# Kernel optimization log

Hardware: AMD Instinct MI355X
Metric: run time of the kernel (lower is better)

Reference implementation:

```python
import jax, jax.numpy as jnp
import numpy as np

EPS = 1e-6

def _feature_map(x):
    # elu(x) + 1 == where(x>0, x+1, exp(x))
    return jax.nn.elu(x) + 1.0

def setup_inputs() -> dict:
    key = jax.random.key(0)
    kq, kk, kv, km = jax.random.split(key, 4)
    B, H, S, D = 4, 16, 4096, 64
    query = jax.random.normal(kq, (B, H, S, D), dtype=jnp.float32)
    key_t = jax.random.normal(kk, (B, H, S, D), dtype=jnp.float32)
    value = jax.random.normal(kv, (B, H, S, D), dtype=jnp.float32)
    # True = padded position
    key_padding_mask = jax.random.bernoulli(km, 0.25, (B, S))
    return {"query": query, "key": key_t, "value": value,
            "key_padding_mask": key_padding_mask}

def reference(query, key, value, key_padding_mask):
    q = _feature_map(query)              # [B,H,S,D]
    k = _feature_map(key)
    v = value
    # valid = ~mask, broadcast over heads and feature dim
    valid = (~key_padding_mask)[:, None, :, None].astype(query.dtype)  # [B,1,S,1]
    k = k * valid
    v = v * valid
    kv = jnp.einsum('bhsd,bhsf->bhdf', k, v)              # [B,H,D,D]
    z = jnp.einsum('bhtd,bhd->bht', q, k.sum(axis=2)) + EPS
    out = jnp.einsum('bhtd,bhdf->bhtf', q, kv) / z[..., None]
    return out
```

## Files before the change

kernel.cpp:

```cpp
#include <hip/hip_runtime.h>

#define S_LEN 4096
#define D_DIM 64
#define NBH   64
#define EPS_F 1e-6f
#define PSZ   (D_DIM * D_DIM + D_DIM)

__device__ __forceinline__ float phi_f(float x) {
    return x > 0.0f ? x + 1.0f : __expf(x);
}

__global__ void detect_mask(const unsigned int* __restrict__ w,
                            unsigned int* __restrict__ flag) {
    __shared__ int all01, allf;
    if (threadIdx.x == 0) { all01 = 1; allf = 1; }
    __syncthreads();
    int a = 1, f = 1;
    for (int i = threadIdx.x; i < 4096; i += blockDim.x) {
        unsigned int v = w[i];
        if (v > 1u) a = 0;
        if (v != 0u && v != 0x3F800000u) f = 0;
    }
    if (!a) atomicExch(&all01, 0);
    if (!f) atomicExch(&allf, 0);
    __syncthreads();
    if (threadIdx.x == 0) *flag = all01 ? 0u : (allf ? 2u : 1u);
}

__global__ __launch_bounds__(256) void la_phase1(
    const float* __restrict__ K, const float* __restrict__ V,
    const void* __restrict__ mask, const unsigned int* __restrict__ flagp,
    float* __restrict__ partials, int CH)
{
    __shared__ float smem[2 * 32 * 64];
    __shared__ float ksred[4][64];

    const int bh   = blockIdx.x;
    const int b    = bh >> 4;
    const unsigned int flag = *flagp;
    const int tid  = threadIdx.x;
    const int wave = tid >> 6;
    const int lane = tid & 63;
    const int tt   = lane >> 3;
    const int tf   = lane & 7;
    const int chunk = S_LEN / CH;
    const int NT    = chunk / 32;
    const int s0    = blockIdx.y * chunk;

    const float* Kbh = K + (size_t)bh * S_LEN * D_DIM;
    const float* Vbh = V + (size_t)bh * S_LEN * D_DIM;
    const int*           mi = (const int*)mask;
    const unsigned char* mb = (const unsigned char*)mask;
    const float*         mf = (const float*)mask;

    float acc[8][8];
    float ks[8];
    #pragma unroll
    for (int i = 0; i < 8; ++i) {
        ks[i] = 0.0f;
        #pragma unroll
        for (int j = 0; j < 8; ++j) acc[i][j] = 0.0f;
    }

    const int row0 = tid >> 4;
    const int col0 = (tid & 15) * 4;

    float4 kr[2], vr[2];
    int    pr[2];

    auto issue = [&](int ts) {
        #pragma unroll
        for (int p = 0; p < 2; ++p) {
            int row = p * 16 + row0;
            int s   = s0 + ts + row;
            int ml  = b * S_LEN + s;
            bool pad;
            if (flag == 0u)      pad = (mi[ml] != 0);
            else if (flag == 1u) pad = (mb[ml] != 0);
            else                 pad = (mf[ml] != 0.0f);
            pr[p] = pad ? 1 : 0;
            kr[p] = *reinterpret_cast<const float4*>(&Kbh[(size_t)s * D_DIM + col0]);
            vr[p] = *reinterpret_cast<const float4*>(&Vbh[(size_t)s * D_DIM + col0]);
        }
    };

    issue(0);
    for (int it = 0; it < NT; ++it) {
        #pragma unroll
        for (int p = 0; p < 2; ++p) {
            int row = p * 16 + row0;
            float4 k4 = kr[p], v4 = vr[p];
            if (pr[p]) {
                k4 = make_float4(0.f, 0.f, 0.f, 0.f);
                v4 = make_float4(0.f, 0.f, 0.f, 0.f);
            } else {
                k4.x = phi_f(k4.x); k4.y = phi_f(k4.y);
                k4.z = phi_f(k4.z); k4.w = phi_f(k4.w);
            }
            *reinterpret_cast<float4*>(&smem[row * 64 + col0])        = k4;
            *reinterpret_cast<float4*>(&smem[2048 + row * 64 + col0]) = v4;
        }
        __syncthreads();
        if (it + 1 < NT) issue((it + 1) * 32);
        #pragma unroll
        for (int r = 0; r < 8; ++r) {
            const int row = wave * 8 + r;
            float kk[8], vv[8];
            *reinterpret_cast<float4*>(&kk[0]) = *reinterpret_cast<const float4*>(&smem[row * 64 + tt * 8]);
            *reinterpret_cast<float4*>(&kk[4]) = *reinterpret_cast<const float4*>(&smem[row * 64 + tt * 8 + 4]);
            *reinterpret_cast<float4*>(&vv[0]) = *reinterpret_cast<const float4*>(&smem[2048 + row * 64 + tf * 8]);
            *reinterpret_cast<float4*>(&vv[4]) = *reinterpret_cast<const float4*>(&smem[2048 + row * 64 + tf * 8 + 4]);
            #pragma unroll
            for (int i = 0; i < 8; ++i) {
                #pragma unroll
                for (int j = 0; j < 8; ++j)
                    acc[i][j] = fmaf(kk[i], vv[j], acc[i][j]);
                ks[i] += kk[i];
            }
        }
        __syncthreads();
    }

    if (tf == 0) {
        #pragma unroll
        for (int i = 0; i < 8; ++i) ksred[wave][tt * 8 + i] = ks[i];
    }
    for (int w = 0; w < 4; ++w) {
        if (wave == w) {
            #pragma unroll
            for (int i = 0; i < 8; ++i) {
                float4* p0 = reinterpret_cast<float4*>(&smem[(tt * 8 + i) * 64 + tf * 8]);
                float4 a0 = make_float4(acc[i][0], acc[i][1], acc[i][2], acc[i][3]);
                float4 a1 = make_float4(acc[i][4], acc[i][5], acc[i][6], acc[i][7]);
                if (w == 0) { p0[0] = a0; p0[1] = a1; }
                else {
                    float4 c0 = p0[0], c1 = p0[1];
                    c0.x += a0.x; c0.y += a0.y; c0.z += a0.z; c0.w += a0.w;
                    c1.x += a1.x; c1.y += a1.y; c1.z += a1.z; c1.w += a1.w;
                    p0[0] = c0; p0[1] = c1;
                }
            }
        }
        __syncthreads();
    }

    float* pp = partials + ((size_t)(bh * CH + blockIdx.y)) * PSZ;
    #pragma unroll
    for (int q = 0; q < 4; ++q) {
        int fi = q * 256 + tid;
        reinterpret_cast<float4*>(pp)[fi] = reinterpret_cast<float4*>(smem)[fi];
    }
    if (tid < 64)
        pp[4096 + tid] = ksred[0][tid] + ksred[1][tid] + ksred[2][tid] + ksred[3][tid];
}

__global__ __launch_bounds__(256) void la_reduce(
    const float* __restrict__ partials, float* __restrict__ kv,
    float* __restrict__ ksum, int CH)
{
    const int bh = blockIdx.x;
    const float4* base = reinterpret_cast<const float4*>(partials + (size_t)bh * CH * PSZ);
    for (int idx = threadIdx.x; idx < PSZ / 4; idx += 256) {
        float4 s = make_float4(0.f, 0.f, 0.f, 0.f);
        for (int c = 0; c < CH; ++c) {
            float4 v = base[(size_t)c * (PSZ / 4) + idx];
            s.x += v.x; s.y += v.y; s.z += v.z; s.w += v.w;
        }
        if (idx < 1024)
            reinterpret_cast<float4*>(kv + (size_t)bh * 4096)[idx] = s;
        else
            reinterpret_cast<float4*>(ksum + bh * 64)[idx - 1024] = s;
    }
}

__global__ __launch_bounds__(128) void la_phase2(
    const float* __restrict__ Q,
    const float* __restrict__ kv_ws, const float* __restrict__ ksum_ws,
    float* __restrict__ out)
{
    __shared__ float qs[2][64][64];
    __shared__ float kvs[64][64];
    __shared__ float kss[64];

    const int bh   = blockIdx.x;
    const int tid  = threadIdx.x;
    const int wave = tid >> 6;
    const int lane = tid & 63;
    const int tt   = lane >> 3;
    const int tf   = lane & 7;
    const int t0   = blockIdx.y * 128;

    const float* Qbh = Q + (size_t)bh * S_LEN * D_DIM;
    const float* kvb = kv_ws + (size_t)bh * D_DIM * D_DIM;

    #pragma unroll
    for (int p = 0; p < 8; ++p) {
        int fi = p * 128 + tid;
        float4 v = *reinterpret_cast<const float4*>(&kvb[fi * 4]);
        *reinterpret_cast<float4*>(&kvs[fi >> 4][(fi & 15) * 4]) = v;
    }
    if (tid < 16)
        reinterpret_cast<float4*>(kss)[tid] =
            reinterpret_cast<const float4*>(ksum_ws + bh * D_DIM)[tid];
    #pragma unroll
    for (int p = 0; p < 16; ++p) {
        int fi = p * 128 + tid;
        int t  = fi >> 4;
        int dq = (fi & 15) * 4;
        float4 qv = *reinterpret_cast<const float4*>(&Qbh[(size_t)(t0 + t) * D_DIM + dq]);
        qv.x = phi_f(qv.x); qv.y = phi_f(qv.y);
        qv.z = phi_f(qv.z); qv.w = phi_f(qv.w);
        int dsw = dq ^ ((t & 7) * 8);
        *reinterpret_cast<float4*>(&qs[t >> 6][t & 63][dsw]) = qv;
    }
    __syncthreads();

    float acc[8][8];
    float z[8];
    #pragma unroll
    for (int r = 0; r < 8; ++r) {
        z[r] = 0.0f;
        #pragma unroll
        for (int c = 0; c < 8; ++c) acc[r][c] = 0.0f;
    }

    #pragma unroll 4
    for (int dq = 0; dq < 64; dq += 4) {
        float ks4[4];
        *reinterpret_cast<float4*>(&ks4[0]) = *reinterpret_cast<const float4*>(&kss[dq]);
        float kvr[4][8];
        #pragma unroll
        for (int j = 0; j < 4; ++j) {
            *reinterpret_cast<float4*>(&kvr[j][0]) = *reinterpret_cast<const float4*>(&kvs[dq + j][tf * 8]);
            *reinterpret_cast<float4*>(&kvr[j][4]) = *reinterpret_cast<const float4*>(&kvs[dq + j][tf * 8 + 4]);
        }
        const int dsw = dq ^ (tt * 8);
        #pragma unroll
        for (int r = 0; r < 8; ++r) {
            float qv[4];
            *reinterpret_cast<float4*>(&qv[0]) =
                *reinterpret_cast<const float4*>(&qs[wave][tt + 8 * r][dsw]);
            z[r] = fmaf(qv[0], ks4[0], fmaf(qv[1], ks4[1],
                   fmaf(qv[2], ks4[2], fmaf(qv[3], ks4[3], z[r]))));
            #pragma unroll
            for (int j = 0; j < 4; ++j)
                #pragma unroll
                for (int c = 0; c < 8; ++c)
                    acc[r][c] = fmaf(qv[j], kvr[j][c], acc[r][c]);
        }
    }

    #pragma unroll
    for (int r = 0; r < 8; ++r) {
        int t = t0 + wave * 64 + tt + 8 * r;
        float inv = 1.0f / (z[r] + EPS_F);
        float o[8];
        #pragma unroll
        for (int c = 0; c < 8; ++c) o[c] = acc[r][c] * inv;
        float* op = out + ((size_t)bh * S_LEN + t) * D_DIM + tf * 8;
        *reinterpret_cast<float4*>(&op[0]) = *reinterpret_cast<const float4*>(&o[0]);
        *reinterpret_cast<float4*>(&op[4]) = *reinterpret_cast<const float4*>(&o[4]);
    }
}

extern "C" void kernel_launch(void* const* d_in, const int* in_sizes, int n_in,
                              void* d_out, int out_size, void* d_ws, size_t ws_size,
                              hipStream_t stream)
{
    (void)in_sizes; (void)n_in; (void)out_size;
    const float* Q   = (const float*)d_in[0];
    const float* K   = (const float*)d_in[1];
    const float* V   = (const float*)d_in[2];
    const void* mask = d_in[3];

    int CH = 16;
    while (CH > 1) {
        size_t need = ((size_t)NBH * CH * PSZ + (size_t)NBH * 4096 + NBH * 64) * 4 + 16;
        if (need <= ws_size) break;
        CH >>= 1;
    }
    float* partials = (float*)d_ws;
    float* kvf  = partials + (size_t)NBH * CH * PSZ;
    float* ksf  = kvf + (size_t)NBH * 4096;
    unsigned int* flag = (unsigned int*)(ksf + NBH * 64);

    detect_mask<<<1, 256, 0, stream>>>((const unsigned int*)mask, flag);
    la_phase1<<<dim3(NBH, CH), 256, 0, stream>>>(K, V, mask, flag, partials, CH);
    la_reduce<<<NBH, 256, 0, stream>>>(partials, kvf, ksf, CH);
    la_phase2<<<dim3(NBH, 32), 128, 0, stream>>>(Q, kvf, ksf, (float*)d_out);
}
```

Baseline: 305.5 us.

## Double-buffer phase1 LDS tiles and stream Q from registers in phase2

Phase1 now uses two shared-memory buffers, so the next tile is transformed and stored while the current one is consumed, removing one barrier per iteration. Phase2 drops its Q staging in shared memory and has each thread read its Q rows straight from global memory with register prefetch. It also moves to 256 threads per block, with 4 rows per thread instead of 8. Launch bounds hint 4 blocks per CU for both kernels. The trade-off is more uncoalesced strided global Q loads and higher LDS use in phase1.

Result: slower. 1.222 ms (+299.9%).

```diff
diff --git a/kernel.cpp b/kernel.cpp
--- a/kernel.cpp
+++ b/kernel.cpp
@@ -27,12 +27,12 @@
     if (threadIdx.x == 0) *flag = all01 ? 0u : (allf ? 2u : 1u);
 }
 
-__global__ __launch_bounds__(256) void la_phase1(
+__global__ __launch_bounds__(256, 4) void la_phase1(
     const float* __restrict__ K, const float* __restrict__ V,
     const void* __restrict__ mask, const unsigned int* __restrict__ flagp,
     float* __restrict__ partials, int CH)
 {
-    __shared__ float smem[2 * 32 * 64];
+    __shared__ float smem[2][4096];
     __shared__ float ksred[4][64];
 
     const int bh   = blockIdx.x;
@@ -84,8 +84,7 @@
         }
     };
 
-    issue(0);
-    for (int it = 0; it < NT; ++it) {
+    auto xstore = [&](int bufi) {
         #pragma unroll
         for (int p = 0; p < 2; ++p) {
             int row = p * 16 + row0;
@@ -97,19 +96,25 @@
                 k4.x = phi_f(k4.x); k4.y = phi_f(k4.y);
                 k4.z = phi_f(k4.z); k4.w = phi_f(k4.w);
             }
-            *reinterpret_cast<float4*>(&smem[row * 64 + col0])        = k4;
-            *reinterpret_cast<float4*>(&smem[2048 + row * 64 + col0]) = v4;
-        }
-        __syncthreads();
+            *reinterpret_cast<float4*>(&smem[bufi][row * 64 + col0])        = k4;
+            *reinterpret_cast<float4*>(&smem[bufi][2048 + row * 64 + col0]) = v4;
+        }
+    };
+
+    issue(0);
+    xstore(0);
+    __syncthreads();
+    int cur = 0;
+    for (int it = 0; it < NT; ++it) {
         if (it + 1 < NT) issue((it + 1) * 32);
         #pragma unroll
         for (int r = 0; r < 8; ++r) {
             const int row = wave * 8 + r;
             float kk[8], vv[8];
-            *reinterpret_cast<float4*>(&kk[0]) = *reinterpret_cast<const float4*>(&smem[row * 64 + tt * 8]);
-            *reinterpret_cast<float4*>(&kk[4]) = *reinterpret_cast<const float4*>(&smem[row * 64 + tt * 8 + 4]);
-            *reinterpret_cast<float4*>(&vv[0]) = *reinterpret_cast<const float4*>(&smem[2048 + row * 64 + tf * 8]);
-            *reinterpret_cast<float4*>(&vv[4]) = *reinterpret_cast<const float4*>(&smem[2048 + row * 64 + tf * 8 + 4]);
+            *reinterpret_cast<float4*>(&kk[0]) = *reinterpret_cast<const float4*>(&smem[cur][row * 64 + tt * 8]);
+            *reinterpret_cast<float4*>(&kk[4]) = *reinterpret_cast<const float4*>(&smem[cur][row * 64 + tt * 8 + 4]);
+            *reinterpret_cast<float4*>(&vv[0]) = *reinterpret_cast<const float4*>(&smem[cur][2048 + row * 64 + tf * 8]);
+            *reinterpret_cast<float4*>(&vv[4]) = *reinterpret_cast<const float4*>(&smem[cur][2048 + row * 64 + tf * 8 + 4]);
             #pragma unroll
             for (int i = 0; i < 8; ++i) {
                 #pragma unroll
@@ -118,7 +123,9 @@
                 ks[i] += kk[i];
             }
         }
+        if (it + 1 < NT) xstore(cur ^ 1);
         __syncthreads();
+        cur ^= 1;
     }
 
     if (tf == 0) {
@@ -129,7 +136,7 @@
         if (wave == w) {
             #pragma unroll
             for (int i = 0; i < 8; ++i) {
-                float4* p0 = reinterpret_cast<float4*>(&smem[(tt * 8 + i) * 64 + tf * 8]);
+                float4* p0 = reinterpret_cast<float4*>(&smem[0][(tt * 8 + i) * 64 + tf * 8]);
                 float4 a0 = make_float4(acc[i][0], acc[i][1], acc[i][2], acc[i][3]);
                 float4 a1 = make_float4(acc[i][4], acc[i][5], acc[i][6], acc[i][7]);
                 if (w == 0) { p0[0] = a0; p0[1] = a1; }
@@ -148,7 +155,7 @@
     #pragma unroll
     for (int q = 0; q < 4; ++q) {
         int fi = q * 256 + tid;
-        reinterpret_cast<float4*>(pp)[fi] = reinterpret_cast<float4*>(smem)[fi];
+        reinterpret_cast<float4*>(pp)[fi] = reinterpret_cast<const float4*>(&smem[0][0])[fi];
     }
     if (tid < 64)
         pp[4096 + tid] = ksred[0][tid] + ksred[1][tid] + ksred[2][tid] + ksred[3][tid];
@@ -173,12 +180,11 @@
     }
 }
 
-__global__ __launch_bounds__(128) void la_phase2(
+__global__ __launch_bounds__(256, 4) void la_phase2(
     const float* __restrict__ Q,
     const float* __restrict__ kv_ws, const float* __restrict__ ksum_ws,
     float* __restrict__ out)
 {
-    __shared__ float qs[2][64][64];
     __shared__ float kvs[64][64];
     __shared__ float kss[64];
 
@@ -188,71 +194,70 @@
     const int lane = tid & 63;
     const int tt   = lane >> 3;
     const int tf   = lane & 7;
-    const int t0   = blockIdx.y * 128;
+    const int t0   = blockIdx.y * 128 + wave * 32;
 
     const float* Qbh = Q + (size_t)bh * S_LEN * D_DIM;
     const float* kvb = kv_ws + (size_t)bh * D_DIM * D_DIM;
 
     #pragma unroll
-    for (int p = 0; p < 8; ++p) {
-        int fi = p * 128 + tid;
-        float4 v = *reinterpret_cast<const float4*>(&kvb[fi * 4]);
-        *reinterpret_cast<float4*>(&kvs[fi >> 4][(fi & 15) * 4]) = v;
+    for (int p = 0; p < 4; ++p) {
+        int fi = p * 256 + tid;
+        reinterpret_cast<float4*>(kvs)[fi] = reinterpret_cast<const float4*>(kvb)[fi];
     }
     if (tid < 16)
         reinterpret_cast<float4*>(kss)[tid] =
             reinterpret_cast<const float4*>(ksum_ws + bh * D_DIM)[tid];
-    #pragma unroll
-    for (int p = 0; p < 16; ++p) {
-        int fi = p * 128 + tid;
-        int t  = fi >> 4;
-        int dq = (fi & 15) * 4;
-        float4 qv = *reinterpret_cast<const float4*>(&Qbh[(size_t)(t0 + t) * D_DIM + dq]);
-        qv.x = phi_f(qv.x); qv.y = phi_f(qv.y);
-        qv.z = phi_f(qv.z); qv.w = phi_f(qv.w);
-        int dsw = dq ^ ((t & 7) * 8);
-        *reinterpret_cast<float4*>(&qs[t >> 6][t & 63][dsw]) = qv;
-    }
-    __syncthreads();
-
-    float acc[8][8];
-    float z[8];
-    #pragma unroll
-    for (int r = 0; r < 8; ++r) {
+    __syncthreads();
+
+    const float* qr0 = Qbh + (size_t)(t0 + tt) * D_DIM;
+
+    float acc[4][8];
+    float z[4];
+    #pragma unroll
+    for (int r = 0; r < 4; ++r) {
         z[r] = 0.0f;
         #pragma unroll
         for (int c = 0; c < 8; ++c) acc[r][c] = 0.0f;
     }
+
+    float4 qn[4];
+    #pragma unroll
+    for (int r = 0; r < 4; ++r)
+        qn[r] = *reinterpret_cast<const float4*>(qr0 + r * 8 * D_DIM);
 
     #pragma unroll 4
     for (int dq = 0; dq < 64; dq += 4) {
+        float qc[4][4];
+        #pragma unroll
+        for (int r = 0; r < 4; ++r) {
+            qc[r][0] = phi_f(qn[r].x); qc[r][1] = phi_f(qn[r].y);
+            qc[r][2] = phi_f(qn[r].z); qc[r][3] = phi_f(qn[r].w);
+        }
+        if (dq + 4 < 64) {
+            #pragma unroll
+            for (int r = 0; r < 4; ++r)
+                qn[r] = *reinterpret_cast<const float4*>(qr0 + r * 8 * D_DIM + dq + 4);
+        }
         float ks4[4];
-        *reinterpret_cast<float4*>(&ks4[0]) = *reinterpret_cast<const float4*>(&kss[dq]);
-        float kvr[4][8];
+        *reinterpret_cast<float4*>(ks4) = *reinterpret_cast<const float4*>(&kss[dq]);
         #pragma unroll
         for (int j = 0; j < 4; ++j) {
-            *reinterpret_cast<float4*>(&kvr[j][0]) = *reinterpret_cast<const float4*>(&kvs[dq + j][tf * 8]);
-            *reinterpret_cast<float4*>(&kvr[j][4]) = *reinterpret_cast<const float4*>(&kvs[dq + j][tf * 8 + 4]);
-        }
-        const int dsw = dq ^ (tt * 8);
-        #pragma unroll
-        for (int r = 0; r < 8; ++r) {
-            float qv[4];
-            *reinterpret_cast<float4*>(&qv[0]) =
-                *reinterpret_cast<const float4*>(&qs[wave][tt + 8 * r][dsw]);
-            z[r] = fmaf(qv[0], ks4[0], fmaf(qv[1], ks4[1],
-                   fmaf(qv[2], ks4[2], fmaf(qv[3], ks4[3], z[r]))));
-            #pragma unroll
-            for (int j = 0; j < 4; ++j)
+            float kvr[8];
+            *reinterpret_cast<float4*>(&kvr[0]) = *reinterpret_cast<const float4*>(&kvs[dq + j][tf * 8]);
+            *reinterpret_cast<float4*>(&kvr[4]) = *reinterpret_cast<const float4*>(&kvs[dq + j][tf * 8 + 4]);
+            #pragma unroll
+            for (int r = 0; r < 4; ++r) {
+                z[r] = fmaf(qc[r][j], ks4[j], z[r]);
                 #pragma unroll
                 for (int c = 0; c < 8; ++c)
-                    acc[r][c] = fmaf(qv[j], kvr[j][c], acc[r][c]);
-        }
-    }
-
-    #pragma unroll
-    for (int r = 0; r < 8; ++r) {
-        int t = t0 + wave * 64 + tt + 8 * r;
+                    acc[r][c] = fmaf(qc[r][j], kvr[c], acc[r][c]);
+            }
+        }
+    }
+
+    #pragma unroll
+    for (int r = 0; r < 4; ++r) {
+        int t = t0 + tt + 8 * r;
         float inv = 1.0f / (z[r] + EPS_F);
         float o[8];
         #pragma unroll
@@ -287,5 +292,5 @@
     detect_mask<<<1, 256, 0, stream>>>((const unsigned int*)mask, flag);
     la_phase1<<<dim3(NBH, CH), 256, 0, stream>>>(K, V, mask, flag, partials, CH);
     la_reduce<<<NBH, 256, 0, stream>>>(partials, kvf, ksf, CH);
-    la_phase2<<<dim3(NBH, 32), 128, 0, stream>>>(Q, kvf, ksf, (float*)d_out);
-}
+    la_phase2<<<dim3(NBH, 32), 256, 0, stream>>>(Q, kvf, ksf, (float*)d_out);
+}
```
